# Performance work log

Hardware: AMD Instinct MI355X
Metric: run time of the kernel (lower is better)

The kernel has to match this reference:

```python
import jax, jax.numpy as jnp
import numpy as np

EPS = 1e-5

def _conv(x, w, b):
    # NCHW, OIHW, stride 1, SAME padding (kernel 3, padding 1)
    y = jax.lax.conv_general_dilated(x, w, (1, 1), 'SAME',
                                     dimension_numbers=('NCHW', 'OIHW', 'NCHW'))
    return y + b[None, :, None, None]

def _maxpool2(x):
    return jax.lax.reduce_window(x, -jnp.inf, jax.lax.max,
                                 (1, 1, 2, 2), (1, 1, 2, 2), 'VALID')

def _fraud_layer(v, theta, phases, sq_r, disp_r, disp_phi, kerr):
    # classical shim of a 2-mode photonic layer; all params are zero -> identity
    c, s = jnp.cos(theta), jnp.sin(theta)
    rot = jnp.array([[1.0, 0.0], [0.0, 1.0]]) * c + jnp.array([[0.0, -1.0], [1.0, 0.0]]) * s
    v = v @ rot.T
    v = v * jnp.cos(phases)          # phase shifters
    v = v * jnp.exp(sq_r)            # squeezing
    v = v + disp_r * jnp.cos(disp_phi)  # displacement
    return v + kerr * v ** 3         # Kerr nonlinearity

def setup_inputs() -> dict:
    key = jax.random.key(0)
    ks = jax.random.split(key, 16)
    B = 4096
    inp = {
        'x': jax.random.normal(ks[0], (B, 1, 32, 32), jnp.float32),
        'conv1_w': jax.random.normal(ks[1], (8, 1, 3, 3), jnp.float32) * 0.2,
        'conv1_b': jnp.zeros((8,), jnp.float32),
        'conv2_w': jax.random.normal(ks[2], (16, 8, 3, 3), jnp.float32) * 0.1,
        'conv2_b': jnp.zeros((16,), jnp.float32),
        'conv3_w': jax.random.normal(ks[3], (32, 16, 3, 3), jnp.float32) * 0.1,
        'conv3_b': jnp.zeros((32,), jnp.float32),
        'gnn_w1': jax.random.normal(ks[4], (32, 32), jnp.float32) * 0.2,
        'gnn_w2': jax.random.normal(ks[5], (16, 32), jnp.float32) * 0.2,
        'rotation_params': jax.random.normal(ks[6], (4, 4), jnp.float32),
        'entangle_params': jax.random.normal(ks[7], (3,), jnp.float32),
        'reduce_w': jax.random.normal(ks[8], (2, 32), jnp.float32) * 0.2,
        'reduce_b': jnp.zeros((2,), jnp.float32),
        'cls_w': jax.random.normal(ks[9], (2, 2), jnp.float32) * 0.5,
        'cls_b': jnp.zeros((2,), jnp.float32),
        'bn_gamma': jnp.ones((2,), jnp.float32),
        'bn_beta': jnp.zeros((2,), jnp.float32),
    }
    return inp

def reference(x, conv1_w, conv1_b, conv2_w, conv2_b, conv3_w, conv3_b,
              gnn_w1, gnn_w2, rotation_params, entangle_params,
              reduce_w, reduce_b, cls_w, cls_b, bn_gamma, bn_beta):
    B = x.shape[0]
    # CNN feature extractor
    h = jax.nn.relu(_conv(x, conv1_w, conv1_b))
    h = _maxpool2(h)
    h = jax.nn.relu(_conv(h, conv2_w, conv2_b))
    h = _maxpool2(h)
    h = jax.nn.relu(_conv(h, conv3_w, conv3_b))
    feats = jnp.mean(h, axis=(2, 3))  # AdaptiveAvgPool2d((1,1)) -> (B, 32)
    # GNN feedforward (batched equivalent of the per-sample Python loop)
    a = jnp.tanh(feats @ gnn_w1.T)    # (B, 32)
    g = jnp.tanh(a @ gnn_w2.T)        # (B, 16)
    # Quantum-style self-attention (runs on detached numpy in original -> stop_gradient)
    d = g.shape[-1]
    q = (g.reshape(B, 4, 4) @ rotation_params).reshape(B, d)
    k = (g.reshape(B, 4, 4) @ rotation_params.T).reshape(B, d)
    temp = jnp.mean(jnp.cos(entangle_params))
    logits = (q @ k.T) * (temp / jnp.sqrt(jnp.asarray(d, jnp.float32)))  # (B, B)
    attn = jax.nn.softmax(logits, axis=-1) @ g                           # (B, 16)
    rep = jnp.concatenate([g, attn], axis=-1)                            # (B, 32)
    rep = jax.lax.stop_gradient(rep)  # numpy round-trip breaks the autograd graph
    # reduce -> fraud layers (all-zero params -> identity) -> classifier
    reduced = rep @ reduce_w.T + reduce_b  # (B, 2)
    z = jnp.zeros((2,), jnp.float32)
    for _ in range(2):  # input layer + 1 hidden layer, all-zero FraudLayerParameters
        reduced = _fraud_layer(reduced, 0.0, z, z, z, z, z)
    out = reduced @ cls_w.T + cls_b  # (B, 2)
    # BatchNorm1d(2) in training mode: batch stats, biased variance
    mu = jnp.mean(out, axis=0)
    var = jnp.mean((out - mu) ** 2, axis=0)
    out = bn_gamma * (out - mu) * jax.lax.rsqrt(var + EPS) + bn_beta
    return out
```

## Files before the change

### kernel.cpp

```cpp
#include <hip/hip_runtime.h>
#include <math.h>

#define LOG2E 1.4426950408889634f

typedef _Float16 h2v __attribute__((ext_vector_type(2)));
typedef _Float16 h4  __attribute__((ext_vector_type(4)));
typedef _Float16 h8  __attribute__((ext_vector_type(8)));
typedef float    f4  __attribute__((ext_vector_type(4)));

__device__ __forceinline__ h2v pk(float a, float b) {
    return __builtin_bit_cast(h2v, __builtin_amdgcn_cvt_pkrtz(a, b));
}

__device__ __forceinline__ f4 mfma16x32(h8 a, h8 b, f4 c) {
    return __builtin_amdgcn_mfma_f32_16x16x32_f16(a, b, c, 0, 0, 0);
}

__device__ __forceinline__ f4 mfma16x16(h4 a, h4 b, f4 c) {
    return __builtin_amdgcn_mfma_f32_16x16x16f16(a, b, c, 0, 0, 0);
}

__device__ __forceinline__ float fast_tanh(float x) {
    const float xc = fminf(fmaxf(x, -15.f), 15.f);
    const float t = exp2f(xc * (2.f * LOG2E));
    return (t - 1.f) * __builtin_amdgcn_rcpf(t + 1.f);
}

__global__ __launch_bounds__(256) void k_pack(
    const float* __restrict__ w1,
    const float* __restrict__ w2, const float* __restrict__ w3,
    _Float16* __restrict__ w2f, _Float16* __restrict__ w3f,
    h2v* __restrict__ w1p, float* __restrict__ w1t)
{
    if (threadIdx.x < 24) {
        const int oc = threadIdx.x / 3, ky = threadIdx.x % 3;
        w1p[threadIdx.x] = pk(w1[oc * 9 + ky * 3 + 0], w1[oc * 9 + ky * 3 + 1]);
        w1t[threadIdx.x] = w1[oc * 9 + ky * 3 + 2];
    }
    for (int idx = threadIdx.x; idx < 1536; idx += 256) {
        const int j = idx & 7;
        const int lane = (idx >> 3) & 63;
        const int c = idx >> 9;
        const int oc = lane & 15;
        const int s = c * 4 + (lane >> 4);
        w2f[idx] = (s < 9) ? (_Float16)w2[oc * 72 + j * 9 + s] : (_Float16)0.f;
    }
    for (int idx = threadIdx.x; idx < 5120; idx += 256) {
        const int j = idx & 7;
        const int lane = (idx >> 3) & 63;
        const int rest = idx >> 9;
        const int mt = rest / 5;
        const int oc = mt * 16 + (lane & 15);
        const int kk = (lane >> 4) * 8 + j;
        const int ic = kk & 15;
        const int sh = (rest - mt * 5) * 2 + (kk >> 4);
        w3f[idx] = (sh < 9) ? (_Float16)w3[oc * 144 + ic * 9 + sh] : (_Float16)0.f;
    }
}

__global__ __launch_bounds__(256) void k_cnn(
    const float* __restrict__ x,
    const h2v* __restrict__ w1p, const float* __restrict__ w1t,
    const float* __restrict__ b1,
    const _Float16* __restrict__ w2f, const float* __restrict__ b2,
    const _Float16* __restrict__ w3f, const float* __restrict__ b3,
    const float* __restrict__ gw1,
    const float* __restrict__ gw2,
    const float* __restrict__ rot,
    const float* __restrict__ ent,
    _Float16* __restrict__ q16, _Float16* __restrict__ k16,
    _Float16* __restrict__ g16, _Float16* __restrict__ gswz)
{
    __shared__ __align__(16) char smem[16384 + 5184 + 3200 + 576 + 128];
    float* xs   = (float*)smem;
    h8*  B2h8   = (h8*)smem;
    h8*  B3full = (h8*)smem;
    h8*  p1c    = (h8*)(smem + 16384);
    h8*  p2hc   = (h8*)(smem + 16384 + 5184);
    h4*  p2h4   = (h4*)(smem + 16384 + 5184);
    float* fsum = (float*)(smem + 16384 + 5184 + 3200);
    float* fs   = fsum + 64;
    float* as   = fs + 32;
    float* gs   = as + 32;
    float* qs   = gs + 16;
    float* ks   = qs + 16;

    const int t = threadIdx.x;
    const int b = blockIdx.x;
    const int lane = t & 63;
    const int w = __builtin_amdgcn_readfirstlane(t >> 6);
    const int nn = lane & 15;
    const int kq = lane >> 4;

    const h8 hzero = (h8)(_Float16)0.f;
    const f4 fzero = {0.f, 0.f, 0.f, 0.f};

    if (t < 132) {
        int r, c;
        if (t < 34)       { r = 0;  c = t; }
        else if (t < 68)  { r = 33; c = t - 34; }
        else if (t < 100) { r = t - 68 + 1;  c = 0; }
        else              { r = t - 100 + 1; c = 33; }
        xs[r * 34 + c] = 0.f;
    } else if (t < 200) {
        const int u = t - 132;
        int r, c;
        if (u < 18)      { r = 0;  c = u; }
        else if (u < 36) { r = 17; c = u - 18; }
        else if (u < 52) { r = u - 36 + 1; c = 0; }
        else             { r = u - 52 + 1; c = 17; }
        p1c[r * 18 + c] = hzero;
    } else if (t < 236) {
        const int u = t - 200;
        int r, c;
        if (u < 10)      { r = 0; c = u; }
        else if (u < 20) { r = 9; c = u - 10; }
        else if (u < 28) { r = u - 20 + 1; c = 0; }
        else             { r = u - 28 + 1; c = 9; }
        p2hc[(r * 10 + c) * 2 + 0] = hzero;
        p2hc[(r * 10 + c) * 2 + 1] = hzero;
    }
    {
        const float4 v = ((const float4*)(x + (size_t)b * 1024))[t];
        const int row = t >> 3;
        const int col = (t & 7) << 2;
        float* dst = &xs[(row + 1) * 34 + col + 1];
        dst[0] = v.x; dst[1] = v.y; dst[2] = v.z; dst[3] = v.w;
    }
    __syncthreads();

    {
        const int px = t & 15, py = t >> 4;
        float pa[4][4];
        #pragma unroll
        for (int iy = 0; iy < 4; ++iy)
            #pragma unroll
            for (int ix = 0; ix < 4; ++ix)
                pa[iy][ix] = xs[(2 * py + iy) * 34 + (2 * px + ix)];
        h2v pA[4], pB[4];
        #pragma unroll
        for (int r = 0; r < 4; ++r) {
            pA[r] = pk(pa[r][0], pa[r][1]);
            pB[r] = pk(pa[r][1], pa[r][2]);
        }

        float r8[8];
        #pragma unroll
        for (int oc = 0; oc < 8; ++oc) {
            const h2v wp0 = w1p[oc * 3 + 0], wp1 = w1p[oc * 3 + 1], wp2 = w1p[oc * 3 + 2];
            const float wt0 = w1t[oc * 3 + 0], wt1 = w1t[oc * 3 + 1], wt2 = w1t[oc * 3 + 2];
            const float bb = b1[oc];
            float mx = -1e30f;
            #pragma unroll
            for (int sy = 0; sy < 2; ++sy) {
                float s0 = bb, s1 = bb;
                s0 = __builtin_amdgcn_fdot2(pA[sy],     wp0, s0, false);
                s0 = __builtin_amdgcn_fdot2(pA[sy + 1], wp1, s0, false);
                s0 = __builtin_amdgcn_fdot2(pA[sy + 2], wp2, s0, false);
                s0 = fmaf(pa[sy][2], wt0, s0);
                s0 = fmaf(pa[sy + 1][2], wt1, s0);
                s0 = fmaf(pa[sy + 2][2], wt2, s0);
                s1 = __builtin_amdgcn_fdot2(pB[sy],     wp0, s1, false);
                s1 = __builtin_amdgcn_fdot2(pB[sy + 1], wp1, s1, false);
                s1 = __builtin_amdgcn_fdot2(pB[sy + 2], wp2, s1, false);
                s1 = fmaf(pa[sy][3], wt0, s1);
                s1 = fmaf(pa[sy + 1][3], wt1, s1);
                s1 = fmaf(pa[sy + 2][3], wt2, s1);
                mx = fmaxf(mx, fmaxf(s0, s1));
            }
            r8[oc] = fmaxf(mx, 0.f);
        }
        union { h8 v; h2v p[4]; } u;
        #pragma unroll
        for (int ocp = 0; ocp < 4; ++ocp) u.p[ocp] = pk(r8[2 * ocp], r8[2 * ocp + 1]);
        p1c[(py + 1) * 18 + (px + 1)] = u.v;
    }

    h8 a2[3];
    #pragma unroll
    for (int c = 0; c < 3; ++c) a2[c] = ((const h8*)w2f)[c * 64 + lane];

    f4 accp[4] = {fzero, fzero, fzero, fzero};
    {
        const int y2 = t >> 4, x2 = t & 15;
        #pragma unroll
        for (int c = 0; c < 3; ++c) {
            __syncthreads();
            #pragma unroll
            for (int sl = 0; sl < 4; ++sl) {
                const int s = c * 4 + sl;
                h8 v = hzero;
                if (s < 9) {
                    const int ky = s / 3, kx = s % 3;
                    v = p1c[(y2 + ky) * 18 + (x2 + kx)];
                }
                B2h8[sl * 256 + t] = v;
            }
            __syncthreads();
            #pragma unroll
            for (int p = 0; p < 4; ++p) {
                const h8 bf = B2h8[kq * 256 + (4 * w + p) * 16 + nn];
                accp[p] = mfma16x32(a2[c], bf, accp[p]);
            }
        }
    }

    {
        float bq[4];
        #pragma unroll
        for (int r = 0; r < 4; ++r) bq[r] = b2[kq * 4 + r];
        #pragma unroll
        for (int i = 0; i < 2; ++i) {
            float m2[4];
            #pragma unroll
            for (int r = 0; r < 4; ++r) {
                const float v0 = fmaxf(accp[2 * i][r] + bq[r], 0.f);
                const float v1 = fmaxf(accp[2 * i + 1][r] + bq[r], 0.f);
                float mv = fmaxf(v0, v1);
                mv = fmaxf(mv, __shfl_xor(mv, 1));
                m2[r] = mv;
            }
            if ((lane & 1) == 0) {
                const int px = nn >> 1;
                const int py = 2 * w + i;
                union { h4 v; h2v p[2]; } u;
                u.p[0] = pk(m2[0], m2[1]);
                u.p[1] = pk(m2[2], m2[3]);
                p2h4[((py + 1) * 10 + (px + 1)) * 4 + kq] = u.v;
            }
        }
    }

    const int mt = w >> 1;
    const int nt0 = (w & 1) * 2;
    h8 a3[5];
    #pragma unroll
    for (int c = 0; c < 5; ++c) a3[c] = ((const h8*)w3f)[(mt * 5 + c) * 64 + lane];

    __syncthreads();
    #pragma unroll
    for (int ss = 0; ss < 5; ++ss) {
        const int idx = ss * 256 + t;
        const int slot = idx >> 6;
        const int pos = idx & 63;
        const int c = slot >> 2;
        const int kq3 = slot & 3;
        const int shv = 2 * c + (kq3 >> 1);
        const int hh = kq3 & 1;
        const int yy = pos >> 3, xx = pos & 7;
        h8 v = hzero;
        if (shv < 9) {
            const int ky = (shv * 11) >> 5;
            const int kx = shv - 3 * ky;
            v = p2hc[((yy + ky) * 10 + (xx + kx)) * 2 + hh];
        }
        B3full[slot * 64 + pos] = v;
    }
    __syncthreads();

    f4 acc3[2] = {fzero, fzero};
    #pragma unroll
    for (int c = 0; c < 5; ++c) {
        #pragma unroll
        for (int p = 0; p < 2; ++p) {
            const h8 bf = B3full[(c * 4 + kq) * 64 + (nt0 + p) * 16 + nn];
            acc3[p] = mfma16x32(a3[c], bf, acc3[p]);
        }
    }

    {
        float bq[4];
        #pragma unroll
        for (int r = 0; r < 4; ++r) bq[r] = b3[mt * 16 + kq * 4 + r];
        float sv[4];
        #pragma unroll
        for (int r = 0; r < 4; ++r) {
            float s = fmaxf(acc3[0][r] + bq[r], 0.f) + fmaxf(acc3[1][r] + bq[r], 0.f);
            #pragma unroll
            for (int off = 1; off < 16; off <<= 1) s += __shfl_xor(s, off);
            sv[r] = s;
        }
        if (nn == 0) {
            const f4 pack = {sv[0], sv[1], sv[2], sv[3]};
            ((f4*)fsum)[mt * 8 + (w & 1) * 4 + kq] = pack;
        }
    }
    __syncthreads();

    if (t < 32)
        fs[t] = (fsum[(t >> 4) * 32 + (t & 15)] +
                 fsum[(t >> 4) * 32 + 16 + (t & 15)]) * (1.f / 64.f);
    __syncthreads();
    if (t < 32) {
        float s = 0.f;
        #pragma unroll
        for (int j = 0; j < 32; ++j) s = fmaf(gw1[t * 32 + j], fs[j], s);
        as[t] = fast_tanh(s);
    }
    __syncthreads();
    if (t < 16) {
        float s = 0.f;
        #pragma unroll
        for (int j = 0; j < 32; ++j) s = fmaf(gw2[t * 32 + j], as[j], s);
        gs[t] = fast_tanh(s);
    }
    __syncthreads();
    if (t < 16) {
        const int r = t >> 2, c = t & 3;
        float qv = 0.f, kv = 0.f;
        #pragma unroll
        for (int j = 0; j < 4; ++j) {
            qv = fmaf(gs[r * 4 + j], rot[j * 4 + c], qv);
            kv = fmaf(gs[r * 4 + j], rot[c * 4 + j], kv);
        }
        qs[t] = qv;
        ks[t] = kv;
    }
    __syncthreads();
    if (t < 8) {
        const float temp = (cosf(ent[0]) + cosf(ent[1]) + cosf(ent[2])) * (1.f / 3.f);
        const float scale = temp * 0.25f;
        ((h2v*)q16)[b * 8 + t] = pk(qs[2 * t] * scale, qs[2 * t + 1] * scale);
        ((h2v*)k16)[b * 8 + t] = pk(ks[2 * t], ks[2 * t + 1]);
        ((h2v*)g16)[b * 8 + t] = pk(gs[2 * t], gs[2 * t + 1]);
    }
    if (t < 16) {
        const int tile = b >> 4, lc = b & 15;
        gswz[tile * 256 + (((lc >> 2) * 16) + t) * 4 + (lc & 3)] = (_Float16)gs[t];
    }
}

__global__ __launch_bounds__(1024) void k_attn(
    const _Float16* __restrict__ q16, const _Float16* __restrict__ k16,
    const _Float16* __restrict__ g16, const _Float16* __restrict__ gswz,
    const float* __restrict__ rw, const float* __restrict__ rb,
    const float* __restrict__ cw, const float* __restrict__ cb,
    float* __restrict__ outp, int B)
{
    __shared__ f4 lO[16][64];
    __shared__ float lm[16][16];
    __shared__ float ll[16][16];

    const int t = threadIdx.x;
    const int lane = t & 63;
    const int w = t >> 6;
    const int rt = blockIdx.x;
    const int r = lane & 15;
    const int q = lane >> 4;
    const f4 fzero = {0.f, 0.f, 0.f, 0.f};

    const h4 qf = *(const h4*)(q16 + ((size_t)(rt * 16 + r)) * 16 + q * 4);

    float m = -1e30f, lp = 0.f;
    f4 O = fzero;

    const int strip = B >> 4;
    const int cbeg = w * strip;
    for (int ci = 0; ci < strip; ci += 16) {
        const int c0 = cbeg + ci;
        const h4 kf = *(const h4*)(k16 + ((size_t)(c0 + r)) * 16 + q * 4);
        const f4 st = mfma16x16(kf, qf, fzero);

        float mx = fmaxf(fmaxf(st[0], st[1]), fmaxf(st[2], st[3]));
        mx = fmaxf(mx, __shfl_xor(mx, 16));
        mx = fmaxf(mx, __shfl_xor(mx, 32));
        if (__ballot(mx > m)) {
            const float mn = fmaxf(m, mx);
            const float a = exp2f((m - mn) * LOG2E);
            lp *= a;
            O[0] *= a; O[1] *= a; O[2] *= a; O[3] *= a;
            m = mn;
        }
        const float p0 = exp2f((st[0] - m) * LOG2E);
        const float p1 = exp2f((st[1] - m) * LOG2E);
        const float p2 = exp2f((st[2] - m) * LOG2E);
        const float p3 = exp2f((st[3] - m) * LOG2E);
        lp += (p0 + p1) + (p2 + p3);

        union { h4 v; h2v p[2]; } u;
        u.p[0] = pk(p0, p1);
        u.p[1] = pk(p2, p3);
        const h4 gf = *(const h4*)(gswz + (size_t)((c0 >> 4)) * 256 + lane * 4);
        O = mfma16x16(gf, u.v, O);
    }
    lp += __shfl_xor(lp, 16);
    lp += __shfl_xor(lp, 32);

    lO[w][lane] = O;
    if (lane < 16) { lm[w][lane] = m; ll[w][lane] = lp; }
    __syncthreads();

    if (w == 0) {
        float M = lm[0][r];
        #pragma unroll
        for (int ww = 1; ww < 16; ++ww) M = fmaxf(M, lm[ww][r]);
        float L = 0.f;
        f4 Om = fzero;
        #pragma unroll
        for (int ww = 0; ww < 16; ++ww) {
            const float f = exp2f((lm[ww][r] - M) * LOG2E);
            L = fmaf(ll[ww][r], f, L);
            const f4 ow = lO[ww][lane];
            Om[0] = fmaf(ow[0], f, Om[0]);
            Om[1] = fmaf(ow[1], f, Om[1]);
            Om[2] = fmaf(ow[2], f, Om[2]);
            Om[3] = fmaf(ow[3], f, Om[3]);
        }
        const float il = 1.f / L;
        const h4 gr = *(const h4*)(g16 + ((size_t)(rt * 16 + r)) * 16 + q * 4);

        float rv[2];
        #pragma unroll
        for (int c = 0; c < 2; ++c) {
            float s = 0.f;
            #pragma unroll
            for (int j = 0; j < 4; ++j) {
                s = fmaf((float)gr[j], rw[c * 32 + q * 4 + j], s);
                s = fmaf(Om[j] * il, rw[c * 32 + 16 + q * 4 + j], s);
            }
            s += __shfl_xor(s, 16);
            s += __shfl_xor(s, 32);
            rv[c] = s + rb[c];
        }
        if (q == 0) {
            float2 o;
            o.x = cb[0] + cw[0] * rv[0] + cw[1] * rv[1];
            o.y = cb[1] + cw[2] * rv[0] + cw[3] * rv[1];
            ((float2*)outp)[rt * 16 + r] = o;
        }
    }
}

__global__ __launch_bounds__(1024) void k_bn(
    float* __restrict__ data, const float* __restrict__ gamma,
    const float* __restrict__ beta, int B)
{
    __shared__ float red[16][4];
    __shared__ float coef[4];
    const int t = threadIdx.x;
    float s0 = 0.f, s1 = 0.f, q0 = 0.f, q1 = 0.f;
    for (int i = t; i < B; i += 1024) {
        const float2 v = ((const float2*)data)[i];
        s0 += v.x; q0 += v.x * v.x;
        s1 += v.y; q1 += v.y * v.y;
    }
    #pragma unroll
    for (int off = 32; off; off >>= 1) {
        s0 += __shfl_xor(s0, off); q0 += __shfl_xor(q0, off);
        s1 += __shfl_xor(s1, off); q1 += __shfl_xor(q1, off);
    }
    if ((t & 63) == 0) {
        red[t >> 6][0] = s0; red[t >> 6][1] = q0;
        red[t >> 6][2] = s1; red[t >> 6][3] = q1;
    }
    __syncthreads();
    if (t == 0) {
        float S0 = 0.f, Q0 = 0.f, S1 = 0.f, Q1 = 0.f;
        for (int w = 0; w < 16; ++w) {
            S0 += red[w][0]; Q0 += red[w][1]; S1 += red[w][2]; Q1 += red[w][3];
        }
        const float inv = 1.f / (float)B;
        const float mu0 = S0 * inv, mu1 = S1 * inv;
        const float v0 = Q0 * inv - mu0 * mu0;
        const float v1 = Q1 * inv - mu1 * mu1;
        const float sc0 = gamma[0] * rsqrtf(v0 + 1e-5f);
        const float sc1 = gamma[1] * rsqrtf(v1 + 1e-5f);
        coef[0] = sc0; coef[1] = beta[0] - mu0 * sc0;
        coef[2] = sc1; coef[3] = beta[1] - mu1 * sc1;
    }
    __syncthreads();
    const float sc0 = coef[0], sh0 = coef[1], sc1 = coef[2], sh1 = coef[3];
    for (int i = t; i < B; i += 1024) {
        float2 v = ((const float2*)data)[i];
        v.x = fmaf(v.x, sc0, sh0);
        v.y = fmaf(v.y, sc1, sh1);
        ((float2*)data)[i] = v;
    }
}

extern "C" void kernel_launch(void* const* d_in, const int* in_sizes, int n_in,
                              void* d_out, int out_size, void* d_ws, size_t ws_size,
                              hipStream_t stream)
{
    (void)n_in; (void)out_size; (void)ws_size;
    const float* x   = (const float*)d_in[0];
    const float* w1  = (const float*)d_in[1];
    const float* b1  = (const float*)d_in[2];
    const float* w2  = (const float*)d_in[3];
    const float* b2  = (const float*)d_in[4];
    const float* w3  = (const float*)d_in[5];
    const float* b3  = (const float*)d_in[6];
    const float* gw1 = (const float*)d_in[7];
    const float* gw2 = (const float*)d_in[8];
    const float* rot = (const float*)d_in[9];
    const float* ent = (const float*)d_in[10];
    const float* rw  = (const float*)d_in[11];
    const float* rbv = (const float*)d_in[12];
    const float* cw  = (const float*)d_in[13];
    const float* cbv = (const float*)d_in[14];
    const float* gam = (const float*)d_in[15];
    const float* bet = (const float*)d_in[16];

    const int B = in_sizes[0] / (32 * 32);

    _Float16* q16  = (_Float16*)d_ws;
    _Float16* k16  = q16 + (size_t)B * 16;
    _Float16* g16  = k16 + (size_t)B * 16;
    _Float16* gswz = g16 + (size_t)B * 16;
    _Float16* w2f  = gswz + (size_t)B * 16;
    _Float16* w3f  = w2f + 1536;
    h2v*      w1p  = (h2v*)(w3f + 5120);
    float*    w1t  = (float*)(w1p + 24);
    float* pre = (float*)d_out;

    k_pack<<<1, 256, 0, stream>>>(w1, w2, w3, w2f, w3f, w1p, w1t);
    k_cnn<<<B, 256, 0, stream>>>(x, w1p, w1t, b1, w2f, b2, w3f, b3, gw1, gw2,
                                 rot, ent, q16, k16, g16, gswz);
    k_attn<<<B / 16, 1024, 0, stream>>>(q16, k16, g16, gswz, rw, rbv, cw, cbv,
                                        pre, B);
    k_bn<<<1, 1024, 0, stream>>>(pre, gam, bet, B);
}
```

Baseline: 142.3 us.

## Read conv2/conv3 MFMA B operands directly from padded LDS instead of im2col staging

Removes the explicit im2col staging buffers for conv2 and conv3. Each lane now loads its MFMA B-fragment straight from the padded pooled feature maps in shared memory, using shift-derived offsets. This drops the copy passes and several __syncthreads barriers and shrinks shared memory, which may allow more resident blocks per CU. In exchange the direct gathers use less regular addresses, so LDS bank conflicts may increase.

```diff
diff --git a/kernel.cpp b/kernel.cpp
--- a/kernel.cpp
+++ b/kernel.cpp
@@ -71,14 +71,12 @@
     _Float16* __restrict__ q16, _Float16* __restrict__ k16,
     _Float16* __restrict__ g16, _Float16* __restrict__ gswz)
 {
-    __shared__ __align__(16) char smem[16384 + 5184 + 3200 + 576 + 128];
+    __shared__ __align__(16) char smem[4624 + 5184 + 3200 + 256 + 512];
     float* xs   = (float*)smem;
-    h8*  B2h8   = (h8*)smem;
-    h8*  B3full = (h8*)smem;
-    h8*  p1c    = (h8*)(smem + 16384);
-    h8*  p2hc   = (h8*)(smem + 16384 + 5184);
-    h4*  p2h4   = (h4*)(smem + 16384 + 5184);
-    float* fsum = (float*)(smem + 16384 + 5184 + 3200);
+    h8*  p1c    = (h8*)(smem + 4624);
+    h8*  p2hc   = (h8*)(smem + 4624 + 5184);
+    h4*  p2h4   = (h4*)(smem + 4624 + 5184);
+    float* fsum = (float*)(smem + 4624 + 5184 + 3200);
     float* fs   = fsum + 64;
     float* as   = fs + 32;
     float* gs   = as + 32;
@@ -180,28 +178,19 @@
     #pragma unroll
     for (int c = 0; c < 3; ++c) a2[c] = ((const h8*)w2f)[c * 64 + lane];
 
+    __syncthreads();
+
     f4 accp[4] = {fzero, fzero, fzero, fzero};
-    {
-        const int y2 = t >> 4, x2 = t & 15;
-        #pragma unroll
-        for (int c = 0; c < 3; ++c) {
-            __syncthreads();
-            #pragma unroll
-            for (int sl = 0; sl < 4; ++sl) {
-                const int s = c * 4 + sl;
-                h8 v = hzero;
-                if (s < 9) {
-                    const int ky = s / 3, kx = s % 3;
-                    v = p1c[(y2 + ky) * 18 + (x2 + kx)];
-                }
-                B2h8[sl * 256 + t] = v;
-            }
-            __syncthreads();
-            #pragma unroll
-            for (int p = 0; p < 4; ++p) {
-                const h8 bf = B2h8[kq * 256 + (4 * w + p) * 16 + nn];
-                accp[p] = mfma16x32(a2[c], bf, accp[p]);
-            }
+    #pragma unroll
+    for (int c = 0; c < 3; ++c) {
+        const int s = c * 4 + kq;
+        const int ky = (s < 9) ? s / 3 : 0;
+        const int kx = (s < 9) ? s % 3 : 0;
+        #pragma unroll
+        for (int p = 0; p < 4; ++p) {
+            h8 bf = hzero;
+            if (s < 9) bf = p1c[(4 * w + p + ky) * 18 + (nn + kx)];
+            accp[p] = mfma16x32(a2[c], bf, accp[p]);
         }
     }
 
@@ -238,32 +227,20 @@
     for (int c = 0; c < 5; ++c) a3[c] = ((const h8*)w3f)[(mt * 5 + c) * 64 + lane];
 
     __syncthreads();
-    #pragma unroll
-    for (int ss = 0; ss < 5; ++ss) {
-        const int idx = ss * 256 + t;
-        const int slot = idx >> 6;
-        const int pos = idx & 63;
-        const int c = slot >> 2;
-        const int kq3 = slot & 3;
-        const int shv = 2 * c + (kq3 >> 1);
-        const int hh = kq3 & 1;
-        const int yy = pos >> 3, xx = pos & 7;
-        h8 v = hzero;
-        if (shv < 9) {
-            const int ky = (shv * 11) >> 5;
-            const int kx = shv - 3 * ky;
-            v = p2hc[((yy + ky) * 10 + (xx + kx)) * 2 + hh];
-        }
-        B3full[slot * 64 + pos] = v;
-    }
-    __syncthreads();
 
     f4 acc3[2] = {fzero, fzero};
     #pragma unroll
     for (int c = 0; c < 5; ++c) {
+        const int shv = 2 * c + (kq >> 1);
+        const int hh = kq & 1;
+        const int ky = (shv < 9) ? ((shv * 11) >> 5) : 0;
+        const int kx = (shv < 9) ? (shv - 3 * ky) : 0;
         #pragma unroll
         for (int p = 0; p < 2; ++p) {
-            const h8 bf = B3full[(c * 4 + kq) * 64 + (nt0 + p) * 16 + nn];
+            const int pos = (nt0 + p) * 16 + nn;
+            const int yy = pos >> 3, xx = pos & 7;
+            h8 bf = hzero;
+            if (shv < 9) bf = p2hc[((yy + ky) * 10 + (xx + kx)) * 2 + hh];
             acc3[p] = mfma16x32(a3[c], bf, acc3[p]);
         }
     }
```

New measurement: 140.2 us. No clear change (-1.5%).
